# Kernel tuning notes

Measured on AMD Instinct MI355X. Metric: run time of the kernel, lower is better.

## Reference

```python
import jax, jax.numpy as jnp
import numpy as np
import math

B, T, D = 8, 1024, 1024
N, L = 256, 768
H = 16
TE = 2048  # time_embed_dim
EPS = 1e-5


def _ln(x, g, b):
    mu = jnp.mean(x, axis=-1, keepdims=True)
    var = jnp.mean(jnp.square(x - mu), axis=-1, keepdims=True)
    return (x - mu) * jax.lax.rsqrt(var + EPS) * g + b


def setup_inputs() -> dict:
    key = jax.random.key(0)
    ks = jax.random.split(key, 16)
    s = lambda fan_in: 1.0 / math.sqrt(fan_in)
    return {
        "x": jax.random.normal(ks[0], (B, T, D), jnp.float32),
        "xf": jax.random.normal(ks[1], (B, N, L), jnp.float32),
        "emb": jax.random.normal(ks[2], (B, TE), jnp.float32),
        "ln_g": jnp.ones((D,), jnp.float32),
        "ln_b": jnp.zeros((D,), jnp.float32),
        "cln_g": jnp.ones((L,), jnp.float32),
        "cln_b": jnp.zeros((L,), jnp.float32),
        "Wq": jax.random.normal(ks[3], (D, D), jnp.float32) * s(D),
        "bq": jnp.zeros((D,), jnp.float32),
        "Wk": jax.random.normal(ks[4], (L, D), jnp.float32) * s(L),
        "bk": jnp.zeros((D,), jnp.float32),
        "Wv": jax.random.normal(ks[5], (L, D), jnp.float32) * s(L),
        "bv": jnp.zeros((D,), jnp.float32),
        "sln_g": jnp.ones((D,), jnp.float32),
        "sln_b": jnp.zeros((D,), jnp.float32),
        "Wemb": jax.random.normal(ks[6], (TE, 2 * D), jnp.float32) * s(TE),
        "bemb": jnp.zeros((2 * D,), jnp.float32),
        "Wout": jax.random.normal(ks[7], (D, D), jnp.float32) * s(D) * 0.02,
        "bout": jnp.zeros((D,), jnp.float32),
    }


def reference(x, xf, emb, ln_g, ln_b, cln_g, cln_b, Wq, bq, Wk, bk, Wv, bv,
              sln_g, sln_b, Wemb, bemb, Wout, bout):
    # x: (B,T,D), xf: (B,N,L), emb: (B,TE)
    hd = D // H
    q = (_ln(x, ln_g, ln_b) @ Wq + bq).reshape(B, T, H, hd)
    xf_n = _ln(xf, cln_g, cln_b)
    k = (xf_n @ Wk + bk).reshape(B, N, H, hd)
    v = (xf_n @ Wv + bv).reshape(B, N, H, hd)
    # scores: (B,T,N,H); note: scaled by sqrt(D//H)
    att = jnp.einsum('bthd,bnhd->btnh', q, k) / math.sqrt(hd)
    w = jax.nn.softmax(att, axis=2)  # softmax over conditioning tokens N
    y = jnp.einsum('btnh,bnhd->bthd', w, v).reshape(B, T, D)
    # StylizationBlock (dropout = 0)
    emb_out = jax.nn.silu(emb) @ Wemb + bemb  # (B, 2D)
    scale, shift = jnp.split(emb_out[:, None, :], 2, axis=2)
    h = _ln(y, sln_g, sln_b) * (1.0 + scale) + shift
    h = jax.nn.silu(h) @ Wout + bout
    return x + h
```

## Files before the change

kernel.cpp:

```cpp
#include <hip/hip_runtime.h>
#include <hip/hip_bf16.h>

typedef __hip_bfloat16 bf16;
typedef unsigned short ushort;
typedef unsigned char uchar;
typedef long i64;
typedef __attribute__((ext_vector_type(4))) float f32x4;

#define B_ 8
#define T_ 1024
#define D_ 1024
#define N_ 256
#define L_ 768
#define H_ 16
#define HD_ 64
#define TE_ 2048

__device__ __forceinline__ void gld16(const void* g, void* l) {
    __builtin_amdgcn_global_load_lds((const __attribute__((address_space(1))) void*)g,
                                     (__attribute__((address_space(3))) void*)l,
                                     16, 0, 0);
}

__device__ __forceinline__ float bitf(unsigned u) { return __uint_as_float(u); }

__device__ __forceinline__ int pk4_fp8(float a, float b, float c, float d) {
    int p = __builtin_amdgcn_cvt_pk_fp8_f32(a, b, 0, false);
    p = __builtin_amdgcn_cvt_pk_fp8_f32(c, d, p, true);
    return p;
}
__device__ __forceinline__ uchar pk1_fp8(float a) {
    int p = __builtin_amdgcn_cvt_pk_fp8_f32(a, a, 0, false);
    return (uchar)(p & 0xff);
}
__device__ __forceinline__ float dec8(uchar b) {
    int e = (b >> 3) & 15, m = b & 7;
    float mag = e ? (float)(8 + m) * bitf((unsigned)(117 + e) << 23)
                  : (float)m * bitf(118u << 23);
    return (b & 0x80) ? -mag : mag;
}

template <int NV>
__device__ __forceinline__ void ln_row(const float* __restrict__ rp,
                                       const float* __restrict__ g,
                                       const float* __restrict__ bb,
                                       uchar* __restrict__ op, int lane) {
    float4 va[NV];
#pragma unroll
    for (int i = 0; i < NV; i++) va[i] = ((const float4*)rp)[i * 64 + lane];
    float s = 0.f, s2 = 0.f;
#pragma unroll
    for (int i = 0; i < NV; i++) {
        s  += va[i].x + va[i].y + va[i].z + va[i].w;
        s2 += va[i].x * va[i].x + va[i].y * va[i].y + va[i].z * va[i].z + va[i].w * va[i].w;
    }
#pragma unroll
    for (int off = 32; off; off >>= 1) {
        s  += __shfl_xor(s,  off, 64);
        s2 += __shfl_xor(s2, off, 64);
    }
    const float inv_n = 1.f / (float)(NV * 256);
    float mu = s * inv_n;
    float var = s2 * inv_n - mu * mu;
    float rstd = rsqrtf(var + 1e-5f);
#pragma unroll
    for (int i = 0; i < NV; i++) {
        float4 gv = ((const float4*)g)[i * 64 + lane];
        float4 bv = ((const float4*)bb)[i * 64 + lane];
        ((int*)op)[i * 64 + lane] = pk4_fp8((va[i].x - mu) * rstd * gv.x + bv.x,
                                            (va[i].y - mu) * rstd * gv.y + bv.y,
                                            (va[i].z - mu) * rstd * gv.z + bv.z,
                                            (va[i].w - mu) * rstd * gv.w + bv.w);
    }
}

__global__ __launch_bounds__(256) void prep_kernel(
        const float* __restrict__ x, const float* __restrict__ xf,
        const float* __restrict__ g1, const float* __restrict__ b1,
        const float* __restrict__ g2, const float* __restrict__ b2,
        const float* __restrict__ Wq, const float* __restrict__ Wk,
        const float* __restrict__ Wv, const float* __restrict__ Wo,
        const float* __restrict__ emb, const float* __restrict__ Wemb,
        uchar* __restrict__ xn8, uchar* __restrict__ xfn8,
        uchar* __restrict__ wq8, uchar* __restrict__ wk8,
        uchar* __restrict__ wv8, uchar* __restrict__ wo8,
        float* __restrict__ part) {
    __shared__ __align__(16) char smem[16384];
    int bid = blockIdx.x;
    int tid = threadIdx.x;
    if (bid < 2560) {
        int w = tid >> 6, lane = tid & 63;
        int row = bid * 4 + w;
        if (row < B_ * T_) {
            ln_row<4>(x + (size_t)row * D_, g1, b1, xn8 + (size_t)row * D_, lane);
        } else {
            int r = row - B_ * T_;
            ln_row<3>(xf + (size_t)r * L_, g2, b2, xfn8 + (size_t)r * L_, lane);
        }
    } else if (bid < 3456) {
        uchar (*t)[65] = (uchar(*)[65])smem;
        int id = bid - 2560;
        int xb = id & 15, y = id >> 4;
        const float* W; uchar* Wt; int K, ky;
        if (y < 16)      { W = Wq; Wt = wq8; K = 1024; ky = y; }
        else if (y < 28) { W = Wk; Wt = wk8; K = 768;  ky = y - 16; }
        else if (y < 40) { W = Wv; Wt = wv8; K = 768;  ky = y - 28; }
        else             { W = Wo; Wt = wo8; K = 1024; ky = y - 40; }
        int k0 = ky * 64, n0 = xb * 64;
#pragma unroll
        for (int i = 0; i < 16; i++) {
            int e = tid + i * 256;
            int r = e >> 6, c = e & 63;
            t[r][c] = pk1_fp8(W[(size_t)(k0 + r) * D_ + n0 + c]);
        }
        __syncthreads();
#pragma unroll
        for (int i = 0; i < 4; i++) {
            int e = tid + i * 256;
            int r = e >> 4, cg = (e & 15) * 4;
            unsigned u = (unsigned)t[cg][r] | ((unsigned)t[cg + 1][r] << 8)
                       | ((unsigned)t[cg + 2][r] << 16) | ((unsigned)t[cg + 3][r] << 24);
            *(unsigned*)&Wt[(size_t)(n0 + r) * K + k0 + cg] = u;
        }
    } else {
        float* se  = (float*)smem;
        float* red = (float*)(smem + 8192);
        int id = bid - 3456;
        int j0 = (id & 31) * 64;
        int ks = id >> 5;
        int tx = tid & 15, ty = tid >> 4;
        int w = tid >> 6, lane = tid & 63;
#pragma unroll
        for (int b = 0; b < 8; b++) {
            float xv = emb[b * TE_ + ks * 256 + tid];
            se[b * 256 + tid] = xv / (1.f + __expf(-xv));
        }
        __syncthreads();
        float acc[8][4] = {};
#pragma unroll 4
        for (int i = 0; i < 16; i++) {
            int e = ty + 16 * i;
            float4 wv = *(const float4*)&Wemb[(size_t)(ks * 256 + e) * 2048 + j0 + tx * 4];
#pragma unroll
            for (int b = 0; b < 8; b++) {
                float s = se[b * 256 + e];
                acc[b][0] += s * wv.x; acc[b][1] += s * wv.y;
                acc[b][2] += s * wv.z; acc[b][3] += s * wv.w;
            }
        }
#pragma unroll
        for (int b = 0; b < 8; b++)
#pragma unroll
            for (int m = 0; m < 4; m++) {
                float v = acc[b][m];
                v += __shfl_down(v, 32, 64);
                v += __shfl_down(v, 16, 64);
                if (lane < 16) red[(w * 8 + b) * 64 + lane * 4 + m] = v;
            }
        __syncthreads();
        for (int o = tid; o < 512; o += 256) {
            int b = o >> 6, jl = o & 63;
            float s = red[(0 * 8 + b) * 64 + jl] + red[(1 * 8 + b) * 64 + jl]
                    + red[(2 * 8 + b) * 64 + jl] + red[(3 * 8 + b) * 64 + jl];
            part[((size_t)ks * 8 + b) * 2048 + j0 + jl] = s;
        }
    }
}

template <int MODE>
__device__ __forceinline__ void gemm_body(const uchar* __restrict__ Ap,
                                          const uchar* __restrict__ Bp,
                                          const float* __restrict__ bias,
                                          const float* __restrict__ res,
                                          void* __restrict__ Cout,
                                          int m0, int n0, int Ncols, int K,
                                          uchar* Ash, uchar* Bsh) {
    int tid = threadIdx.x;
    int w = tid >> 6, lane = tid & 63;
    int quad = lane >> 4, l15 = lane & 15;
    int wm = (w >> 1) * 64, wn = (w & 1) * 64;
    int lr4 = lane >> 2;
    int sp4 = lane & 3;
    f32x4 acc[4][4] = {};
    for (int kt = 0; kt < K; kt += 64) {
#pragma unroll
        for (int j = 0; j < 2; j++) {
            int r = w * 32 + j * 16 + lr4;
            int gc = sp4 ^ (r & 3);
            gld16(&Ap[(size_t)(m0 + r) * K + kt + gc * 16], &Ash[(w * 32 + j * 16) * 64]);
        }
#pragma unroll
        for (int j = 0; j < 2; j++) {
            int r = w * 32 + j * 16 + lr4;
            int gc = sp4 ^ (r & 3);
            gld16(&Bp[(size_t)(n0 + r) * K + kt + gc * 16], &Bsh[(w * 32 + j * 16) * 64]);
        }
        __syncthreads();
#pragma unroll
        for (int kh = 0; kh < 2; kh++) {
            int c4 = kh * 2 + (quad >> 1);
            int sub = (quad & 1) * 8;
            int pos = (c4 ^ (l15 & 3)) * 16 + sub;
            i64 af[4], bfr[4];
#pragma unroll
            for (int mt = 0; mt < 4; mt++)
                af[mt] = *(const i64*)&Ash[(wm + mt * 16 + l15) * 64 + pos];
#pragma unroll
            for (int nt = 0; nt < 4; nt++)
                bfr[nt] = *(const i64*)&Bsh[(wn + nt * 16 + l15) * 64 + pos];
#pragma unroll
            for (int mt = 0; mt < 4; mt++)
#pragma unroll
                for (int nt = 0; nt < 4; nt++)
                    acc[mt][nt] = __builtin_amdgcn_mfma_f32_16x16x32_fp8_fp8(af[mt], bfr[nt], acc[mt][nt], 0, 0, 0);
        }
        __syncthreads();
    }
    if (MODE == 0) {
#pragma unroll
        for (int mt = 0; mt < 4; mt++)
#pragma unroll
            for (int nt = 0; nt < 4; nt++)
#pragma unroll
                for (int reg = 0; reg < 4; reg++) {
                    int rl = wm + mt * 16 + quad * 4 + reg;
                    int cl = wn + nt * 16 + l15;
                    Ash[rl * 128 + cl] = pk1_fp8(acc[mt][nt][reg] + bias[n0 + cl]);
                }
        __syncthreads();
#pragma unroll
        for (int i = 0; i < 4; i++) {
            int row = (tid >> 3) + i * 32;
            int ch = (tid & 7) * 16;
            *(int4*)&((uchar*)Cout)[(size_t)(m0 + row) * Ncols + n0 + ch] =
                *(const int4*)&Ash[row * 128 + ch];
        }
    } else {
#pragma unroll
        for (int mt = 0; mt < 4; mt++) {
#pragma unroll
            for (int nt = 0; nt < 4; nt++) {
#pragma unroll
                for (int reg = 0; reg < 4; reg++) {
                    int row = m0 + wm + mt * 16 + quad * 4 + reg;
                    int col = n0 + wn + nt * 16 + l15;
                    float v = acc[mt][nt][reg] + bias[col];
                    if (MODE == 1) {
                        v += res[(size_t)row * Ncols + col];
                        ((float*)Cout)[(size_t)row * Ncols + col] = v;
                    } else {
                        int b = row >> 8, n = row & 255;
                        int h = col >> 6, d = col & 63;
                        size_t addr = ((size_t)(b * 16 + h)) * 16384 + (size_t)d * 256
                                    + (((n >> 4) ^ (d & 15)) * 16) + (n & 15);
                        ((uchar*)Cout)[addr] = pk1_fp8(v);
                    }
                }
            }
        }
    }
}

__global__ __launch_bounds__(256, 4) void qkv_gemm(const uchar* __restrict__ xn8,
                                                   const uchar* __restrict__ xfn8,
                                                   const uchar* __restrict__ wq8,
                                                   const uchar* __restrict__ wk8,
                                                   const uchar* __restrict__ wv8,
                                                   const float* __restrict__ bq,
                                                   const float* __restrict__ bk,
                                                   const float* __restrict__ bv,
                                                   uchar* __restrict__ q8,
                                                   uchar* __restrict__ k8,
                                                   uchar* __restrict__ vT8,
                                                   const float* __restrict__ part,
                                                   const float* __restrict__ bemb,
                                                   float* __restrict__ embo) {
    __shared__ __align__(16) uchar SH[16384];
    int bid = blockIdx.x;
    if (bid < 512) {
        gemm_body<0>(xn8, wq8, bq, nullptr, q8,
                     (bid & 63) * 128, (bid >> 6) * 128, D_, D_, SH, SH + 8192);
    } else if (bid < 640) {
        int id = bid - 512;
        gemm_body<0>(xfn8, wk8, bk, nullptr, k8,
                     (id & 15) * 128, (id >> 4) * 128, D_, L_, SH, SH + 8192);
    } else if (bid < 768) {
        int id = bid - 640;
        gemm_body<2>(xfn8, wv8, bv, nullptr, vT8,
                     (id & 15) * 128, (id >> 4) * 128, D_, L_, SH, SH + 8192);
    } else {
        int o = (bid - 768) * 256 + threadIdx.x;
        int b = o >> 11, j = o & 2047;
        float s = bemb[j];
#pragma unroll
        for (int ks = 0; ks < 8; ks++) s += part[((size_t)ks * 8 + b) * 2048 + j];
        embo[o] = s;
    }
}

__global__ __launch_bounds__(256, 4) void out_gemm(const uchar* __restrict__ a8,
                                                   const uchar* __restrict__ wo8,
                                                   const float* __restrict__ bout,
                                                   const float* __restrict__ x,
                                                   float* __restrict__ out) {
    __shared__ __align__(16) uchar SH[16384];
    int bid = blockIdx.x;
    gemm_body<1>(a8, wo8, bout, x, out,
                 (bid & 63) * 128, (bid >> 6) * 128, D_, D_, SH, SH + 8192);
}

__global__ __launch_bounds__(256) void attn_mfma(const uchar* __restrict__ q8,
                                                 const uchar* __restrict__ k8,
                                                 const uchar* __restrict__ vT8,
                                                 uchar* __restrict__ y8) {
    __shared__ __align__(16) uchar KV[16384];
    __shared__ __align__(16) uchar P[16384];
    int tid = threadIdx.x;
    int w = tid >> 6, lane = tid & 63;
    int quad = lane >> 4, l15 = lane & 15;
    int bid = blockIdx.x;
    int work = (bid & 7) * 256 + (bid >> 3);
    int t0 = (work & 15) * 64;
    int bh = work >> 4;
    int b = bh >> 4, h = bh & 15;
    int lln = lane >> 3, sp = lane & 7;

#pragma unroll 1
    for (int rep = 0; rep < 3; rep++) {
#pragma unroll
        for (int j = 0; j < 4; j++) {
            int dn = w * 32 + j * 8 + lln;
            int c8 = sp ^ (dn & 7);
            int n = dn * 2 + (c8 >> 2);
            gld16(&k8[(size_t)(b * N_ + n) * D_ + h * 64 + (c8 & 3) * 16],
                  &KV[(w * 32 + j * 8) * 128]);
        }
#pragma unroll
        for (int j = 0; j < 2; j++) {
            int r = w * 16 + j * 8 + lln;
            int c = (sp ^ (r & 7)) & 3;
            gld16(&q8[(size_t)(b * T_ + t0 + r) * D_ + h * 64 + c * 16],
                  &P[(w * 16 + j * 8) * 128]);
        }
        __syncthreads();

        int qrow = w * 16 + l15;
        i64 aq[2];
#pragma unroll
        for (int kk2 = 0; kk2 < 2; kk2++) {
            int chunk = kk2 * 2 + (quad >> 1);
            aq[kk2] = *(const i64*)&P[qrow * 128 + ((chunk ^ (qrow & 7)) * 16) + (quad & 1) * 8];
        }
        f32x4 sf[16];
#pragma unroll
        for (int nt = 0; nt < 16; nt++) {
            int n = nt * 16 + l15;
            int dn = n >> 1, hn = n & 1;
            int c80 = (hn * 4 + 0 + (quad >> 1)) ^ (dn & 7);
            int c81 = (hn * 4 + 2 + (quad >> 1)) ^ (dn & 7);
            i64 b0 = *(const i64*)&KV[dn * 128 + c80 * 16 + (quad & 1) * 8];
            i64 b1 = *(const i64*)&KV[dn * 128 + c81 * 16 + (quad & 1) * 8];
            f32x4 z = {};
            f32x4 t = __builtin_amdgcn_mfma_f32_16x16x32_fp8_fp8(aq[0], b0, z, 0, 0, 0);
            sf[nt] = __builtin_amdgcn_mfma_f32_16x16x32_fp8_fp8(aq[1], b1, t, 0, 0, 0);
        }
        __syncthreads();

        const uchar* vbase = vT8 + (size_t)(b * 16 + h) * 16384;
#pragma unroll
        for (int j = 0; j < 4; j++) {
            gld16(&vbase[(w * 4 + j) * 1024 + lane * 16], &KV[(w * 4 + j) * 1024]);
        }

        const float scale = 0.125f;
        float sm[4] = {0.f, 0.f, 0.f, 0.f};
#pragma unroll
        for (int nt = 0; nt < 16; nt++)
#pragma unroll
            for (int reg = 0; reg < 4; reg++) {
                float e = __expf(sf[nt][reg] * scale);
                sf[nt][reg] = e;
                sm[reg] += e;
            }
#pragma unroll
        for (int off = 1; off < 16; off <<= 1)
#pragma unroll
            for (int reg = 0; reg < 4; reg++)
                sm[reg] += __shfl_xor(sm[reg], off, 64);
        float inv[4];
#pragma unroll
        for (int reg = 0; reg < 4; reg++) inv[reg] = 1.f / sm[reg];

#pragma unroll
        for (int nt = 0; nt < 16; nt++)
#pragma unroll
            for (int reg = 0; reg < 4; reg++) {
                int r = w * 16 + quad * 4 + reg;
                int n = nt * 16 + l15;
                P[r * 256 + (((n >> 4) ^ (r & 15)) * 16) + (n & 15)] = pk1_fp8(sf[nt][reg]);
            }
        __syncthreads();

        f32x4 of[4] = {};
        int prow = w * 16 + l15;
#pragma unroll
        for (int kk = 0; kk < 8; kk++) {
            int ck = kk * 2 + (quad >> 1);
            i64 ap = *(const i64*)&P[prow * 256 + ((ck ^ (prow & 15)) * 16) + (quad & 1) * 8];
#pragma unroll
            for (int dt = 0; dt < 4; dt++) {
                int d = dt * 16 + l15;
                i64 bv = *(const i64*)&KV[d * 256 + ((ck ^ (d & 15)) * 16) + (quad & 1) * 8];
                of[dt] = __builtin_amdgcn_mfma_f32_16x16x32_fp8_fp8(ap, bv, of[dt], 0, 0, 0);
            }
        }
        __syncthreads();
#pragma unroll
        for (int dt = 0; dt < 4; dt++)
#pragma unroll
            for (int reg = 0; reg < 4; reg++) {
                int rl = w * 16 + quad * 4 + reg;
                P[rl * 64 + dt * 16 + l15] = pk1_fp8(of[dt][reg] * inv[reg]);
            }
        __syncthreads();
        {
            int row = tid >> 2, ch = (tid & 3) * 16;
            *(int4*)&y8[(size_t)(b * T_ + t0 + row) * D_ + h * 64 + ch] =
                *(const int4*)&P[row * 64 + ch];
        }
        __syncthreads();
    }
}

__global__ __launch_bounds__(256) void styl_kernel(const uchar* __restrict__ y8,
                                                   const float* __restrict__ g,
                                                   const float* __restrict__ bb,
                                                   const float* __restrict__ embo,
                                                   uchar* __restrict__ a8) {
    int tid = threadIdx.x, w = tid >> 6, lane = tid & 63;
    int row = blockIdx.x * 4 + w;
    int b = row >> 10;
    const uchar* rp = y8 + (size_t)row * D_;
    uchar* op = a8 + (size_t)row * D_;
    float v[16];
    float s = 0.f, s2 = 0.f;
#pragma unroll
    for (int i = 0; i < 4; i++) {
        unsigned u = ((const unsigned*)rp)[i * 64 + lane];
#pragma unroll
        for (int j = 0; j < 4; j++) {
            float f = dec8((uchar)(u >> (8 * j)));
            v[i * 4 + j] = f; s += f; s2 += f * f;
        }
    }
#pragma unroll
    for (int off = 32; off; off >>= 1) {
        s  += __shfl_xor(s,  off, 64);
        s2 += __shfl_xor(s2, off, 64);
    }
    float mu = s * (1.f / 1024.f);
    float rstd = rsqrtf(s2 * (1.f / 1024.f) - mu * mu + 1e-5f);
#pragma unroll
    for (int i = 0; i < 4; i++) {
        int c4 = i * 64 + lane;
        float4 gv  = ((const float4*)g)[c4];
        float4 bv  = ((const float4*)bb)[c4];
        float4 scv = ((const float4*)(embo + b * 2048))[c4];
        float4 shv = ((const float4*)(embo + b * 2048 + 1024))[c4];
        float h0 = (v[i*4+0] - mu) * rstd * gv.x + bv.x;
        float h1 = (v[i*4+1] - mu) * rstd * gv.y + bv.y;
        float h2 = (v[i*4+2] - mu) * rstd * gv.z + bv.z;
        float h3 = (v[i*4+3] - mu) * rstd * gv.w + bv.w;
        h0 = h0 * (1.f + scv.x) + shv.x;
        h1 = h1 * (1.f + scv.y) + shv.y;
        h2 = h2 * (1.f + scv.z) + shv.z;
        h3 = h3 * (1.f + scv.w) + shv.w;
        h0 = h0 / (1.f + __expf(-h0));
        h1 = h1 / (1.f + __expf(-h1));
        h2 = h2 / (1.f + __expf(-h2));
        h3 = h3 / (1.f + __expf(-h3));
        ((int*)op)[c4] = pk4_fp8(h0, h1, h2, h3);
    }
}

extern "C" void kernel_launch(void* const* d_in, const int* in_sizes, int n_in,
                              void* d_out, int out_size, void* d_ws, size_t ws_size,
                              hipStream_t stream) {
    const float* x    = (const float*)d_in[0];
    const float* xf   = (const float*)d_in[1];
    const float* emb  = (const float*)d_in[2];
    const float* ln_g = (const float*)d_in[3];
    const float* ln_b = (const float*)d_in[4];
    const float* cln_g= (const float*)d_in[5];
    const float* cln_b= (const float*)d_in[6];
    const float* Wq   = (const float*)d_in[7];
    const float* bq   = (const float*)d_in[8];
    const float* Wk   = (const float*)d_in[9];
    const float* bk   = (const float*)d_in[10];
    const float* Wv   = (const float*)d_in[11];
    const float* bv   = (const float*)d_in[12];
    const float* sln_g= (const float*)d_in[13];
    const float* sln_b= (const float*)d_in[14];
    const float* Wemb = (const float*)d_in[15];
    const float* bemb = (const float*)d_in[16];
    const float* Wout = (const float*)d_in[17];
    const float* bout = (const float*)d_in[18];
    float* out = (float*)d_out;

    char* wsp = (char*)d_ws;
    const size_t MB = 1024 * 1024;
    uchar* xn8  = (uchar*)(wsp);
    uchar* xfn8 = (uchar*)(wsp + 8 * MB);
    uchar* wq8  = (uchar*)(wsp + 10 * MB);
    uchar* wk8  = (uchar*)(wsp + 11 * MB);
    uchar* wv8  = (uchar*)(wsp + 12 * MB);
    uchar* wo8  = (uchar*)(wsp + 13 * MB);
    uchar* q8   = (uchar*)(wsp + 14 * MB);
    uchar* k8   = (uchar*)(wsp + 22 * MB);
    uchar* vT8  = (uchar*)(wsp + 24 * MB);
    uchar* y8   = (uchar*)(wsp + 26 * MB);
    uchar* a8   = (uchar*)(wsp + 34 * MB);
    float* embo = (float*)(wsp + 42 * MB);
    float* part = (float*)(wsp + 43 * MB);

    prep_kernel<<<3712, 256, 0, stream>>>(x, xf, ln_g, ln_b, cln_g, cln_b,
                                          Wq, Wk, Wv, Wout, emb, Wemb,
                                          xn8, xfn8, wq8, wk8, wv8, wo8, part);

    qkv_gemm<<<832, 256, 0, stream>>>(xn8, xfn8, wq8, wk8, wv8, bq, bk, bv,
                                      q8, k8, vT8, part, bemb, embo);

    attn_mfma<<<2048, 256, 0, stream>>>(q8, k8, vT8, y8);

    styl_kernel<<<2048, 256, 0, stream>>>(y8, sln_g, sln_b, embo, a8);

    out_gemm<<<512, 256, 0, stream>>>(a8, wo8, bout, x, out);
}
```

Measured before the change: 274.2 us.

## Double-buffer FP8 GEMM tiles and remove triplicated attention loop

The shared GEMM body now uses two LDS buffers, issuing the async global-to-LDS loads for the next K tile while MFMAs run on the current one. This halves the number of block barriers per tile pair. LDS per GEMM block doubles to 32 KB, which can affect occupancy, and the loop now assumes an even number of K tiles. The attention kernel also drops an outer loop that repeated the identical attention computation three times, removing redundant work.

```diff
diff --git a/kernel.cpp b/kernel.cpp
--- a/kernel.cpp
+++ b/kernel.cpp
@@ -174,28 +174,34 @@
                                           const float* __restrict__ res,
                                           void* __restrict__ Cout,
                                           int m0, int n0, int Ncols, int K,
-                                          uchar* Ash, uchar* Bsh) {
+                                          uchar* SH) {
     int tid = threadIdx.x;
     int w = tid >> 6, lane = tid & 63;
     int quad = lane >> 4, l15 = lane & 15;
     int wm = (w >> 1) * 64, wn = (w & 1) * 64;
     int lr4 = lane >> 2;
     int sp4 = lane & 3;
+    uchar* A0 = SH;
+    uchar* B0 = SH + 8192;
+    uchar* A1 = SH + 16384;
+    uchar* B1 = SH + 24576;
     f32x4 acc[4][4] = {};
-    for (int kt = 0; kt < K; kt += 64) {
+
+    auto stage = [&](int kt, uchar* As, uchar* Bs) {
 #pragma unroll
         for (int j = 0; j < 2; j++) {
             int r = w * 32 + j * 16 + lr4;
             int gc = sp4 ^ (r & 3);
-            gld16(&Ap[(size_t)(m0 + r) * K + kt + gc * 16], &Ash[(w * 32 + j * 16) * 64]);
+            gld16(&Ap[(size_t)(m0 + r) * K + kt + gc * 16], &As[(w * 32 + j * 16) * 64]);
         }
 #pragma unroll
         for (int j = 0; j < 2; j++) {
             int r = w * 32 + j * 16 + lr4;
             int gc = sp4 ^ (r & 3);
-            gld16(&Bp[(size_t)(n0 + r) * K + kt + gc * 16], &Bsh[(w * 32 + j * 16) * 64]);
-        }
-        __syncthreads();
+            gld16(&Bp[(size_t)(n0 + r) * K + kt + gc * 16], &Bs[(w * 32 + j * 16) * 64]);
+        }
+    };
+    auto compute = [&](const uchar* As, const uchar* Bs) {
 #pragma unroll
         for (int kh = 0; kh < 2; kh++) {
             int c4 = kh * 2 + (quad >> 1);
@@ -204,18 +210,30 @@
             i64 af[4], bfr[4];
 #pragma unroll
             for (int mt = 0; mt < 4; mt++)
-                af[mt] = *(const i64*)&Ash[(wm + mt * 16 + l15) * 64 + pos];
+                af[mt] = *(const i64*)&As[(wm + mt * 16 + l15) * 64 + pos];
 #pragma unroll
             for (int nt = 0; nt < 4; nt++)
-                bfr[nt] = *(const i64*)&Bsh[(wn + nt * 16 + l15) * 64 + pos];
+                bfr[nt] = *(const i64*)&Bs[(wn + nt * 16 + l15) * 64 + pos];
 #pragma unroll
             for (int mt = 0; mt < 4; mt++)
 #pragma unroll
                 for (int nt = 0; nt < 4; nt++)
                     acc[mt][nt] = __builtin_amdgcn_mfma_f32_16x16x32_fp8_fp8(af[mt], bfr[nt], acc[mt][nt], 0, 0, 0);
         }
+    };
+
+    int nt2 = K >> 6;
+    stage(0, A0, B0);
+    __syncthreads();
+    for (int t = 0; t + 2 <= nt2; t += 2) {
+        stage((t + 1) * 64, A1, B1);
+        compute(A0, B0);
         __syncthreads();
-    }
+        if (t + 2 < nt2) stage((t + 2) * 64, A0, B0);
+        compute(A1, B1);
+        __syncthreads();
+    }
+
     if (MODE == 0) {
 #pragma unroll
         for (int mt = 0; mt < 4; mt++)
@@ -225,7 +243,7 @@
                 for (int reg = 0; reg < 4; reg++) {
                     int rl = wm + mt * 16 + quad * 4 + reg;
                     int cl = wn + nt * 16 + l15;
-                    Ash[rl * 128 + cl] = pk1_fp8(acc[mt][nt][reg] + bias[n0 + cl]);
+                    SH[rl * 128 + cl] = pk1_fp8(acc[mt][nt][reg] + bias[n0 + cl]);
                 }
         __syncthreads();
 #pragma unroll
@@ -233,7 +251,7 @@
             int row = (tid >> 3) + i * 32;
             int ch = (tid & 7) * 16;
             *(int4*)&((uchar*)Cout)[(size_t)(m0 + row) * Ncols + n0 + ch] =
-                *(const int4*)&Ash[row * 128 + ch];
+                *(const int4*)&SH[row * 128 + ch];
         }
     } else {
 #pragma unroll
@@ -275,19 +293,19 @@
                                                    const float* __restrict__ part,
                                                    const float* __restrict__ bemb,
                                                    float* __restrict__ embo) {
-    __shared__ __align__(16) uchar SH[16384];
+    __shared__ __align__(16) uchar SH[32768];
     int bid = blockIdx.x;
     if (bid < 512) {
         gemm_body<0>(xn8, wq8, bq, nullptr, q8,
-                     (bid & 63) * 128, (bid >> 6) * 128, D_, D_, SH, SH + 8192);
+                     (bid & 63) * 128, (bid >> 6) * 128, D_, D_, SH);
     } else if (bid < 640) {
         int id = bid - 512;
         gemm_body<0>(xfn8, wk8, bk, nullptr, k8,
-                     (id & 15) * 128, (id >> 4) * 128, D_, L_, SH, SH + 8192);
+                     (id & 15) * 128, (id >> 4) * 128, D_, L_, SH);
     } else if (bid < 768) {
         int id = bid - 640;
         gemm_body<2>(xfn8, wv8, bv, nullptr, vT8,
-                     (id & 15) * 128, (id >> 4) * 128, D_, L_, SH, SH + 8192);
+                     (id & 15) * 128, (id >> 4) * 128, D_, L_, SH);
     } else {
         int o = (bid - 768) * 256 + threadIdx.x;
         int b = o >> 11, j = o & 2047;
@@ -303,10 +321,10 @@
                                                    const float* __restrict__ bout,
                                                    const float* __restrict__ x,
                                                    float* __restrict__ out) {
-    __shared__ __align__(16) uchar SH[16384];
+    __shared__ __align__(16) uchar SH[32768];
     int bid = blockIdx.x;
     gemm_body<1>(a8, wo8, bout, x, out,
-                 (bid & 63) * 128, (bid >> 6) * 128, D_, D_, SH, SH + 8192);
+                 (bid & 63) * 128, (bid >> 6) * 128, D_, D_, SH);
 }
 
 __global__ __launch_bounds__(256) void attn_mfma(const uchar* __restrict__ q8,
@@ -325,110 +343,106 @@
     int b = bh >> 4, h = bh & 15;
     int lln = lane >> 3, sp = lane & 7;
 
-#pragma unroll 1
-    for (int rep = 0; rep < 3; rep++) {
-#pragma unroll
-        for (int j = 0; j < 4; j++) {
-            int dn = w * 32 + j * 8 + lln;
-            int c8 = sp ^ (dn & 7);
-            int n = dn * 2 + (c8 >> 2);
-            gld16(&k8[(size_t)(b * N_ + n) * D_ + h * 64 + (c8 & 3) * 16],
-                  &KV[(w * 32 + j * 8) * 128]);
-        }
-#pragma unroll
-        for (int j = 0; j < 2; j++) {
-            int r = w * 16 + j * 8 + lln;
-            int c = (sp ^ (r & 7)) & 3;
-            gld16(&q8[(size_t)(b * T_ + t0 + r) * D_ + h * 64 + c * 16],
-                  &P[(w * 16 + j * 8) * 128]);
-        }
-        __syncthreads();
-
-        int qrow = w * 16 + l15;
-        i64 aq[2];
-#pragma unroll
-        for (int kk2 = 0; kk2 < 2; kk2++) {
-            int chunk = kk2 * 2 + (quad >> 1);
-            aq[kk2] = *(const i64*)&P[qrow * 128 + ((chunk ^ (qrow & 7)) * 16) + (quad & 1) * 8];
-        }
-        f32x4 sf[16];
-#pragma unroll
-        for (int nt = 0; nt < 16; nt++) {
+#pragma unroll
+    for (int j = 0; j < 4; j++) {
+        int dn = w * 32 + j * 8 + lln;
+        int c8 = sp ^ (dn & 7);
+        int n = dn * 2 + (c8 >> 2);
+        gld16(&k8[(size_t)(b * N_ + n) * D_ + h * 64 + (c8 & 3) * 16],
+              &KV[(w * 32 + j * 8) * 128]);
+    }
+#pragma unroll
+    for (int j = 0; j < 2; j++) {
+        int r = w * 16 + j * 8 + lln;
+        int c = (sp ^ (r & 7)) & 3;
+        gld16(&q8[(size_t)(b * T_ + t0 + r) * D_ + h * 64 + c * 16],
+              &P[(w * 16 + j * 8) * 128]);
+    }
+    __syncthreads();
+
+    int qrow = w * 16 + l15;
+    i64 aq[2];
+#pragma unroll
+    for (int kk2 = 0; kk2 < 2; kk2++) {
+        int chunk = kk2 * 2 + (quad >> 1);
+        aq[kk2] = *(const i64*)&P[qrow * 128 + ((chunk ^ (qrow & 7)) * 16) + (quad & 1) * 8];
+    }
+    f32x4 sf[16];
+#pragma unroll
+    for (int nt = 0; nt < 16; nt++) {
+        int n = nt * 16 + l15;
+        int dn = n >> 1, hn = n & 1;
+        int c80 = (hn * 4 + 0 + (quad >> 1)) ^ (dn & 7);
+        int c81 = (hn * 4 + 2 + (quad >> 1)) ^ (dn & 7);
+        i64 b0 = *(const i64*)&KV[dn * 128 + c80 * 16 + (quad & 1) * 8];
+        i64 b1 = *(const i64*)&KV[dn * 128 + c81 * 16 + (quad & 1) * 8];
+        f32x4 z = {};
+        f32x4 t = __builtin_amdgcn_mfma_f32_16x16x32_fp8_fp8(aq[0], b0, z, 0, 0, 0);
+        sf[nt] = __builtin_amdgcn_mfma_f32_16x16x32_fp8_fp8(aq[1], b1, t, 0, 0, 0);
+    }
+    __syncthreads();
+
+    const uchar* vbase = vT8 + (size_t)(b * 16 + h) * 16384;
+#pragma unroll
+    for (int j = 0; j < 4; j++) {
+        gld16(&vbase[(w * 4 + j) * 1024 + lane * 16], &KV[(w * 4 + j) * 1024]);
+    }
+
+    const float scale = 0.125f;
+    float sm[4] = {0.f, 0.f, 0.f, 0.f};
+#pragma unroll
+    for (int nt = 0; nt < 16; nt++)
+#pragma unroll
+        for (int reg = 0; reg < 4; reg++) {
+            float e = __expf(sf[nt][reg] * scale);
+            sf[nt][reg] = e;
+            sm[reg] += e;
+        }
+#pragma unroll
+    for (int off = 1; off < 16; off <<= 1)
+#pragma unroll
+        for (int reg = 0; reg < 4; reg++)
+            sm[reg] += __shfl_xor(sm[reg], off, 64);
+    float inv[4];
+#pragma unroll
+    for (int reg = 0; reg < 4; reg++) inv[reg] = 1.f / sm[reg];
+
+#pragma unroll
+    for (int nt = 0; nt < 16; nt++)
+#pragma unroll
+        for (int reg = 0; reg < 4; reg++) {
+            int r = w * 16 + quad * 4 + reg;
             int n = nt * 16 + l15;
-            int dn = n >> 1, hn = n & 1;
-            int c80 = (hn * 4 + 0 + (quad >> 1)) ^ (dn & 7);
-            int c81 = (hn * 4 + 2 + (quad >> 1)) ^ (dn & 7);
-            i64 b0 = *(const i64*)&KV[dn * 128 + c80 * 16 + (quad & 1) * 8];
-            i64 b1 = *(const i64*)&KV[dn * 128 + c81 * 16 + (quad & 1) * 8];
-            f32x4 z = {};
-            f32x4 t = __builtin_amdgcn_mfma_f32_16x16x32_fp8_fp8(aq[0], b0, z, 0, 0, 0);
-            sf[nt] = __builtin_amdgcn_mfma_f32_16x16x32_fp8_fp8(aq[1], b1, t, 0, 0, 0);
-        }
-        __syncthreads();
-
-        const uchar* vbase = vT8 + (size_t)(b * 16 + h) * 16384;
-#pragma unroll
-        for (int j = 0; j < 4; j++) {
-            gld16(&vbase[(w * 4 + j) * 1024 + lane * 16], &KV[(w * 4 + j) * 1024]);
-        }
-
-        const float scale = 0.125f;
-        float sm[4] = {0.f, 0.f, 0.f, 0.f};
-#pragma unroll
-        for (int nt = 0; nt < 16; nt++)
-#pragma unroll
-            for (int reg = 0; reg < 4; reg++) {
-                float e = __expf(sf[nt][reg] * scale);
-                sf[nt][reg] = e;
-                sm[reg] += e;
-            }
-#pragma unroll
-        for (int off = 1; off < 16; off <<= 1)
-#pragma unroll
-            for (int reg = 0; reg < 4; reg++)
-                sm[reg] += __shfl_xor(sm[reg], off, 64);
-        float inv[4];
-#pragma unroll
-        for (int reg = 0; reg < 4; reg++) inv[reg] = 1.f / sm[reg];
-
-#pragma unroll
-        for (int nt = 0; nt < 16; nt++)
-#pragma unroll
-            for (int reg = 0; reg < 4; reg++) {
-                int r = w * 16 + quad * 4 + reg;
-                int n = nt * 16 + l15;
-                P[r * 256 + (((n >> 4) ^ (r & 15)) * 16) + (n & 15)] = pk1_fp8(sf[nt][reg]);
-            }
-        __syncthreads();
-
-        f32x4 of[4] = {};
-        int prow = w * 16 + l15;
-#pragma unroll
-        for (int kk = 0; kk < 8; kk++) {
-            int ck = kk * 2 + (quad >> 1);
-            i64 ap = *(const i64*)&P[prow * 256 + ((ck ^ (prow & 15)) * 16) + (quad & 1) * 8];
-#pragma unroll
-            for (int dt = 0; dt < 4; dt++) {
-                int d = dt * 16 + l15;
-                i64 bv = *(const i64*)&KV[d * 256 + ((ck ^ (d & 15)) * 16) + (quad & 1) * 8];
-                of[dt] = __builtin_amdgcn_mfma_f32_16x16x32_fp8_fp8(ap, bv, of[dt], 0, 0, 0);
-            }
-        }
-        __syncthreads();
-#pragma unroll
-        for (int dt = 0; dt < 4; dt++)
-#pragma unroll
-            for (int reg = 0; reg < 4; reg++) {
-                int rl = w * 16 + quad * 4 + reg;
-                P[rl * 64 + dt * 16 + l15] = pk1_fp8(of[dt][reg] * inv[reg]);
-            }
-        __syncthreads();
-        {
-            int row = tid >> 2, ch = (tid & 3) * 16;
-            *(int4*)&y8[(size_t)(b * T_ + t0 + row) * D_ + h * 64 + ch] =
-                *(const int4*)&P[row * 64 + ch];
-        }
-        __syncthreads();
+            P[r * 256 + (((n >> 4) ^ (r & 15)) * 16) + (n & 15)] = pk1_fp8(sf[nt][reg]);
+        }
+    __syncthreads();
+
+    f32x4 of[4] = {};
+    int prow = w * 16 + l15;
+#pragma unroll
+    for (int kk = 0; kk < 8; kk++) {
+        int ck = kk * 2 + (quad >> 1);
+        i64 ap = *(const i64*)&P[prow * 256 + ((ck ^ (prow & 15)) * 16) + (quad & 1) * 8];
+#pragma unroll
+        for (int dt = 0; dt < 4; dt++) {
+            int d = dt * 16 + l15;
+            i64 bv = *(const i64*)&KV[d * 256 + ((ck ^ (d & 15)) * 16) + (quad & 1) * 8];
+            of[dt] = __builtin_amdgcn_mfma_f32_16x16x32_fp8_fp8(ap, bv, of[dt], 0, 0, 0);
+        }
+    }
+    __syncthreads();
+#pragma unroll
+    for (int dt = 0; dt < 4; dt++)
+#pragma unroll
+        for (int reg = 0; reg < 4; reg++) {
+            int rl = w * 16 + quad * 4 + reg;
+            P[rl * 64 + dt * 16 + l15] = pk1_fp8(of[dt][reg] * inv[reg]);
+        }
+    __syncthreads();
+    {
+        int row = tid >> 2, ch = (tid & 3) * 16;
+        *(int4*)&y8[(size_t)(b * T_ + t0 + row) * D_ + h * 64 + ch] =
+            *(const int4*)&P[row * 64 + ch];
     }
 }
 
```

New measurement: 233.8 us. 14.7% less time.
